# Kernel optimization log

Measured on AMD Instinct MI355X. Metric: run time of the kernel, lower is better.

Reference implementation:

```python
import jax, jax.numpy as jnp
import numpy as np

L_IN, L_K = 1, 1            # degree ranges (0..L)
C_IN, K_CH, H = 16, 8, 4    # in_channels, k_channels (per head), num_heads
C_OUT = H * K_CH            # 32
E, N_NODES, EMB = 32768, 4096, 64
M_IN, M_K = (L_IN + 1) ** 2, (L_K + 1) ** 2


def _so2_pairs(L_in, L_out):
    # enumerate SO(2)-equivariant weight blocks: for each order m, all (l_in, l_out)
    # pairs with l >= m; m=0 uses 1 matrix, m>0 uses 2 (real/imag parts).
    pairs, w = [], 0
    for m in range(min(L_in, L_out) + 1):
        for l_in in range(m, L_in + 1):
            for l_out in range(m, L_out + 1):
                pairs.append((m, l_in, l_out, w))
                w += 1 if m == 0 else 2
    return pairs, w

_PAIRS, NUM_W = _so2_pairs(L_IN, L_K)  # NUM_W = 6 for L_in=L_k=1


def so2_linear(x, W, L_in, L_out):
    # x: [E, (L_in+1)^2, Cin]; W: [NUM_W, Cin, Cout] (shared) or [E, NUM_W, Cin, Cout] (per-edge)
    per_edge = (W.ndim == 4)
    Cout = W.shape[-1]
    out = jnp.zeros((x.shape[0], (L_out + 1) ** 2, Cout), x.dtype)

    def mat(xs, w):
        return jnp.einsum('ec,eco->eo', xs, W[:, w]) if per_edge else xs @ W[w]

    pairs, _ = _so2_pairs(L_in, L_out)
    for m, l_in, l_out, w in pairs:
        i_in, i_out = l_in * (l_in + 1), l_out * (l_out + 1)  # flat index of (l, m=0)
        if m == 0:
            out = out.at[:, i_out].add(mat(x[:, i_in], w))
        else:
            xp, xn = x[:, i_in + m], x[:, i_in - m]
            out = out.at[:, i_out + m].add(mat(xp, w) - mat(xn, w + 1))
            out = out.at[:, i_out - m].add(mat(xp, w + 1) + mat(xn, w))
    return out


def segment_softmax(z, index, num_segments):
    # PyG-style softmax over ragged neighborhoods (max is detached, as in PyG)
    zmax = jax.lax.stop_gradient(jax.ops.segment_max(z, index, num_segments=num_segments))
    e = jnp.exp(z - zmax[index])
    denom = jax.ops.segment_sum(e, index, num_segments=num_segments)
    return e / denom[index]


def setup_inputs() -> dict:
    key = jax.random.key(0)
    ks = jax.random.split(key, 6)
    x_q = jax.random.normal(ks[0], (E, M_IN, C_IN), jnp.float32)
    x_k = jax.random.normal(ks[1], (E, M_IN, C_IN), jnp.float32)
    edge_emb = jax.random.normal(ks[2], (E, EMB), jnp.float32)
    index = jnp.sort(jax.random.randint(ks[3], (E,), 0, N_NODES))
    W_q = jax.random.normal(ks[4], (NUM_W, C_IN, C_OUT), jnp.float32) / np.sqrt(C_IN)
    W_p = jax.random.normal(ks[5], (EMB, NUM_W * C_IN * C_OUT), jnp.float32) / np.sqrt(EMB)
    return {"x_q": x_q, "x_k": x_k, "edge_emb": edge_emb, "index": index,
            "W_q": W_q, "W_p": W_p, "num_nodes": N_NODES}


def reference(x_q, x_k, edge_emb, index, W_q, W_p, num_nodes):
    # q_ij = W_Q x_i ; static SO2 weights
    q = so2_linear(x_q, W_q, L_IN, L_K).reshape(-1, M_K, H, K_CH)
    # k_ij = W_K(||r_ij||) x_j ; per-edge dynamic SO2 weights from edge embedding
    W_k = (edge_emb @ W_p).reshape(-1, NUM_W, C_IN, C_OUT)
    k = so2_linear(x_k, W_k, L_IN, L_K).reshape(-1, M_K, H, K_CH)
    scale = (K_CH // H) ** (-0.5)  # faithful to original: (k_channels // num_heads)**-0.5
    z = (q * k).sum((-1, -3)) * scale  # [E, H]
    return segment_softmax(z, index, num_nodes)
```

## Files before the change

### kernel.cpp

```cpp
#include <hip/hip_runtime.h>
#include <math.h>

#define E_TOTAL 32768
#define NUM_NODES 4096
#define SCALE 0.70710678118654752f

typedef __attribute__((ext_vector_type(8))) short bfrag;
typedef __attribute__((ext_vector_type(16))) float facc;

__device__ inline unsigned short f2bf(float f) {
  unsigned int u = __float_as_uint(f);
  unsigned int r = (u + 0x7FFFu + ((u >> 16) & 1u)) >> 16;
  return (unsigned short)r;
}
__device__ inline float bf2f(unsigned short s) {
  return __uint_as_float(((unsigned int)s) << 16);
}
__device__ inline void cvt8(const float* v, bfrag& hi, bfrag& lo) {
#pragma unroll
  for (int i = 0; i < 8; ++i) {
    unsigned short h = f2bf(v[i]);
    hi[i] = (short)h;
    lo[i] = (short)f2bf(v[i] - bf2f(h));
  }
}

__global__ __launch_bounds__(256) void prep_kernel(
    const float* __restrict__ Wp, const float* __restrict__ Wq,
    const int* __restrict__ index,
    unsigned short* __restrict__ fragWp, unsigned short* __restrict__ fragWq,
    int* __restrict__ offs)
{
  const int b = blockIdx.x, t = threadIdx.x;
  if (b < 96) {
    __shared__ unsigned short lds[4096];
    const int c = b / 6, w = b - c * 6;
    const int colbase = w * 512 + c * 32;
    const int cl = t & 31, dg = t >> 5;
#pragma unroll
    for (int i = 0; i < 8; ++i) {
      const int d = dg * 8 + i;
      const float v = Wp[(size_t)d * 3072 + colbase + cl];
      const unsigned short hi = f2bf(v);
      const unsigned short lo = f2bf(v - bf2f(hi));
      const int ks = d >> 4;
      const int lane = ((d >> 3) & 1) * 32 + cl;
      const int j = d & 7;
      lds[(ks * 2 + 0) * 512 + lane * 8 + j] = hi;
      lds[(ks * 2 + 1) * 512 + lane * 8 + j] = lo;
    }
    __syncthreads();
    unsigned short* dst = fragWp + (size_t)b * 4096;
    ((uint4*)dst)[t] = ((const uint4*)lds)[t];
    ((uint4*)dst)[t + 256] = ((const uint4*)lds)[t + 256];
  } else if (b < 103) {
    const int slot = b - 96;
    const int w = (slot == 6) ? 5 : slot;
    const float sgn = (slot == 6) ? -1.f : 1.f;
    for (int tt = t; tt < 512; tt += 256) {
      const int lane = tt >> 3, j = tt & 7;
      const int o = lane & 31, c = (lane >> 5) * 8 + j;
      const float v = sgn * Wq[(size_t)(w * 16 + c) * 32 + o];
      const unsigned short hi = f2bf(v);
      const unsigned short lo = f2bf(v - bf2f(hi));
      fragWq[slot * 1024 + lane * 8 + j] = hi;
      fragWq[slot * 1024 + 512 + lane * 8 + j] = lo;
    }
  } else {
    const int tg = (b - 103) * 256 + t;
    if (tg >= E_TOTAL) return;
    const int cur = index[tg];
    const int prev = (tg == 0) ? -1 : index[tg - 1];
    for (int n = prev + 1; n <= cur; ++n) offs[n] = tg;
    if (tg == E_TOTAL - 1)
      for (int n = cur + 1; n <= NUM_NODES; ++n) offs[n] = E_TOTAL;
  }
}

__global__ __launch_bounds__(256, 2) void main_kernel(
    const float* __restrict__ x_q, const float* __restrict__ x_k,
    const float* __restrict__ emb,
    const unsigned short* __restrict__ fragWp,
    const unsigned short* __restrict__ fragWq,
    float* __restrict__ z)
{
  __shared__ float xk_t[64][65];
  __shared__ float zred[4][32][4];

  const int t = threadIdx.x;
  const int lane = t & 63, wv = t >> 6;
  const int pr = wv & 1;
  const int col = lane & 31, half = lane >> 5;
  const int eb = blockIdx.x * 64;
  const int el = (wv >> 1) * 32 + col;
  const int e = eb + el;

  {
    const int er = t >> 2, dq = (t & 3) * 16;
    const float* src = x_k + (size_t)(eb + er) * 64 + dq;
#pragma unroll
    for (int i = 0; i < 4; ++i) {
      float4 v = *(const float4*)(src + i * 4);
      xk_t[dq + i * 4 + 0][er] = v.x;
      xk_t[dq + i * 4 + 1][er] = v.y;
      xk_t[dq + i * 4 + 2][er] = v.z;
      xk_t[dq + i * 4 + 3][er] = v.w;
    }
  }

  bfrag ebh[4], ebl[4];
#pragma unroll
  for (int ks = 0; ks < 4; ++ks) {
    float tmp[8];
    *(float4*)&tmp[0] = *(const float4*)(emb + (size_t)e * 64 + ks * 16 + half * 8);
    *(float4*)&tmp[4] = *(const float4*)(emb + (size_t)e * 64 + ks * 16 + half * 8 + 4);
    cvt8(tmp, ebh[ks], ebl[ks]);
  }

  facc ka0 = {0}, ka1 = {0}, ka2 = {0}, ka3 = {0};

  const unsigned short* fbase = fragWp + pr * 4096 + lane * 8;

  bfrag curh[4], curl[4], nxth[4], nxtl[4];
#pragma unroll
  for (int ks = 0; ks < 4; ++ks) {
    *(uint4*)&curh[ks] = *(const uint4*)(fbase + ks * 1024);
    *(uint4*)&curl[ks] = *(const uint4*)(fbase + ks * 1024 + 512);
  }

  __syncthreads();

  float xkc0 = 0.f, xkc1 = 0.f, xkc2 = 0.f, xkc3 = 0.f;

#pragma unroll 6
  for (int it = 0; it < 48; ++it) {
    const int j = it % 3;
    {
      const int itn = (it < 47) ? it + 1 : 47;
      const unsigned short* gp = fbase + (size_t)itn * 8192;
#pragma unroll
      for (int ks = 0; ks < 4; ++ks) {
        *(uint4*)&nxth[ks] = *(const uint4*)(gp + ks * 1024);
        *(uint4*)&nxtl[ks] = *(const uint4*)(gp + ks * 1024 + 512);
      }
    }
    if (j == 0) {
      const int c16 = it / 3;
      xkc0 = xk_t[c16][el];
      xkc1 = xk_t[16 + c16][el];
      xkc2 = xk_t[32 + c16][el];
      xkc3 = xk_t[48 + c16][el];
    }
    facc cc0 = {0.f}, cc1 = {0.f}, cc2 = {0.f};
#pragma unroll
    for (int ks = 0; ks < 4; ++ks) {
      cc0 = __builtin_amdgcn_mfma_f32_32x32x16_bf16(curh[ks], ebh[ks], cc0, 0, 0, 0);
      cc1 = __builtin_amdgcn_mfma_f32_32x32x16_bf16(curh[ks], ebl[ks], cc1, 0, 0, 0);
      cc2 = __builtin_amdgcn_mfma_f32_32x32x16_bf16(curl[ks], ebh[ks], cc2, 0, 0, 0);
    }
    if (j < 2) {
      const float xv = (j == 0) ? xkc0 : xkc2;
      if (pr == 0) {
#pragma unroll
        for (int r = 0; r < 16; ++r)
          ka0[r] = fmaf(xv, cc0[r] + cc1[r] + cc2[r], ka0[r]);
      } else {
#pragma unroll
        for (int r = 0; r < 16; ++r)
          ka2[r] = fmaf(xv, cc0[r] + cc1[r] + cc2[r], ka2[r]);
      }
    } else {
      if (pr == 0) {
#pragma unroll
        for (int r = 0; r < 16; ++r) {
          const float s = cc0[r] + cc1[r] + cc2[r];
          ka1[r] = fmaf(xkc1, s, ka1[r]);
          ka3[r] = fmaf(xkc3, s, ka3[r]);
        }
      } else {
#pragma unroll
        for (int r = 0; r < 16; ++r) {
          const float s = cc0[r] + cc1[r] + cc2[r];
          ka1[r] = fmaf(xkc3, s, ka1[r]);
          ka3[r] = fmaf(-xkc1, s, ka3[r]);
        }
      }
    }
#pragma unroll
    for (int ks = 0; ks < 4; ++ks) { curh[ks] = nxth[ks]; curl[ks] = nxtl[ks]; }
  }

  bfrag xqh[4], xql[4];
#pragma unroll
  for (int a = 0; a < 4; ++a) {
    float tmp[8];
    *(float4*)&tmp[0] = *(const float4*)(x_q + (size_t)e * 64 + a * 16 + half * 8);
    *(float4*)&tmp[4] = *(const float4*)(x_q + (size_t)e * 64 + a * 16 + half * 8 + 4);
    cvt8(tmp, xqh[a], xql[a]);
  }
  float zp0 = 0.f, zp1 = 0.f, zp2 = 0.f, zp3 = 0.f;
  const int QA1[4] = {0, 1, 0, 3}, QS1[4] = {0, 4, 1, 4};
  const int QA2[4] = {2, 3, 2, 1}, QS2[4] = {2, 5, 3, 6};
#pragma unroll
  for (int m = 0; m < 4; ++m) {
    facc qa = {0.f};
#pragma unroll
    for (int tm = 0; tm < 2; ++tm) {
      const int a = tm ? QA2[m] : QA1[m];
      const int sl = tm ? QS2[m] : QS1[m];
      bfrag wh, wl;
      *(uint4*)&wh = *(const uint4*)(fragWq + sl * 1024 + lane * 8);
      *(uint4*)&wl = *(const uint4*)(fragWq + sl * 1024 + 512 + lane * 8);
      qa = __builtin_amdgcn_mfma_f32_32x32x16_bf16(wh, xqh[a], qa, 0, 0, 0);
      qa = __builtin_amdgcn_mfma_f32_32x32x16_bf16(wh, xql[a], qa, 0, 0, 0);
      qa = __builtin_amdgcn_mfma_f32_32x32x16_bf16(wl, xqh[a], qa, 0, 0, 0);
    }
    const facc& km = (m == 0) ? ka0 : (m == 1) ? ka1 : (m == 2) ? ka2 : ka3;
#pragma unroll
    for (int r = 0; r < 16; ++r) {
      const float v = qa[r] * km[r];
      if (r < 4) zp0 += v;
      else if (r < 8) zp1 += v;
      else if (r < 12) zp2 += v;
      else zp3 += v;
    }
  }
  zp0 += __shfl_xor(zp0, 32);
  zp1 += __shfl_xor(zp1, 32);
  zp2 += __shfl_xor(zp2, 32);
  zp3 += __shfl_xor(zp3, 32);
  if (half == 0) {
    float4 v = {zp0, zp1, zp2, zp3};
    *(float4*)&zred[wv][col][0] = v;
  }
  __syncthreads();
  if (pr == 0 && half == 0) {
    float4 a = *(const float4*)&zred[wv][col][0];
    float4 b = *(const float4*)&zred[wv ^ 1][col][0];
    float4 o = {(a.x + b.x) * SCALE, (a.y + b.y) * SCALE,
                (a.z + b.z) * SCALE, (a.w + b.w) * SCALE};
    *(float4*)&z[(size_t)e * 4] = o;
  }
}

__global__ __launch_bounds__(256) void softmax_kernel(
    const float* __restrict__ z, const int* __restrict__ offs,
    float* __restrict__ out)
{
  const int node = blockIdx.x * 4 + (threadIdx.x >> 6);
  const int lane = threadIdx.x & 63;
  const int start = offs[node], end = offs[node + 1];
  if (start >= end) return;
  const int h = lane & 3, eo = lane >> 2;
  float m = -INFINITY;
  for (int e = start + eo; e < end; e += 16) m = fmaxf(m, z[(size_t)e * 4 + h]);
#pragma unroll
  for (int s = 4; s < 64; s <<= 1) m = fmaxf(m, __shfl_xor(m, s));
  float sum = 0.f;
  for (int e = start + eo; e < end; e += 16) sum += __expf(z[(size_t)e * 4 + h] - m);
#pragma unroll
  for (int s = 4; s < 64; s <<= 1) sum += __shfl_xor(sum, s);
  const float inv = 1.f / sum;
  for (int e = start + eo; e < end; e += 16)
    out[(size_t)e * 4 + h] = __expf(z[(size_t)e * 4 + h] - m) * inv;
}

extern "C" void kernel_launch(void* const* d_in, const int* in_sizes, int n_in,
                              void* d_out, int out_size, void* d_ws, size_t ws_size,
                              hipStream_t stream) {
  const float* x_q = (const float*)d_in[0];
  const float* x_k = (const float*)d_in[1];
  const float* emb = (const float*)d_in[2];
  const int* index = (const int*)d_in[3];
  const float* W_q = (const float*)d_in[4];
  const float* W_p = (const float*)d_in[5];
  float* out = (float*)d_out;

  char* ws = (char*)d_ws;
  float* z = (float*)ws;
  int* offs = (int*)(ws + 524288);
  unsigned short* fragWp = (unsigned short*)(ws + 524288 + 32768);
  unsigned short* fragWq = (unsigned short*)(ws + 524288 + 32768 + 786432);

  prep_kernel<<<231, 256, 0, stream>>>(W_p, W_q, index, fragWp, fragWq, offs);
  main_kernel<<<512, 256, 0, stream>>>(x_q, x_k, emb, fragWp, fragWq, z);
  softmax_kernel<<<1024, 256, 0, stream>>>(z, offs, out);
}
```

Measured before the change: 123.9 us.

## Split per-edge weight channel loop across eight waves and drop offsets pass

Doubles the main kernel block to 512 threads. Each wave pair now covers all 32 output columns for 32 edges, and four wave groups split the 16 input channels among them, so each wave runs 24 iterations instead of 48. Partial z values are reduced across the four groups through shared memory. Separately, the segment-offset computation is removed from the prep kernel and the softmax kernel finds each node's edge range by binary search on the sorted index. This adds redundant index reads and a larger cross-wave reduction, and raises register pressure under the 512x4 launch bounds.

```diff
diff --git a/kernel.cpp b/kernel.cpp
--- a/kernel.cpp
+++ b/kernel.cpp
@@ -27,9 +27,7 @@
 
 __global__ __launch_bounds__(256) void prep_kernel(
     const float* __restrict__ Wp, const float* __restrict__ Wq,
-    const int* __restrict__ index,
-    unsigned short* __restrict__ fragWp, unsigned short* __restrict__ fragWq,
-    int* __restrict__ offs)
+    unsigned short* __restrict__ fragWp, unsigned short* __restrict__ fragWq)
 {
   const int b = blockIdx.x, t = threadIdx.x;
   if (b < 96) {
@@ -53,7 +51,7 @@
     unsigned short* dst = fragWp + (size_t)b * 4096;
     ((uint4*)dst)[t] = ((const uint4*)lds)[t];
     ((uint4*)dst)[t + 256] = ((const uint4*)lds)[t + 256];
-  } else if (b < 103) {
+  } else {
     const int slot = b - 96;
     const int w = (slot == 6) ? 5 : slot;
     const float sgn = (slot == 6) ? -1.f : 1.f;
@@ -66,18 +64,10 @@
       fragWq[slot * 1024 + lane * 8 + j] = hi;
       fragWq[slot * 1024 + 512 + lane * 8 + j] = lo;
     }
-  } else {
-    const int tg = (b - 103) * 256 + t;
-    if (tg >= E_TOTAL) return;
-    const int cur = index[tg];
-    const int prev = (tg == 0) ? -1 : index[tg - 1];
-    for (int n = prev + 1; n <= cur; ++n) offs[n] = tg;
-    if (tg == E_TOTAL - 1)
-      for (int n = cur + 1; n <= NUM_NODES; ++n) offs[n] = E_TOTAL;
-  }
-}
-
-__global__ __launch_bounds__(256, 2) void main_kernel(
+  }
+}
+
+__global__ __launch_bounds__(512, 4) void main_kernel(
     const float* __restrict__ x_q, const float* __restrict__ x_k,
     const float* __restrict__ emb,
     const unsigned short* __restrict__ fragWp,
@@ -85,27 +75,25 @@
     float* __restrict__ z)
 {
   __shared__ float xk_t[64][65];
-  __shared__ float zred[4][32][4];
+  __shared__ float zred[8][32][4];
 
   const int t = threadIdx.x;
   const int lane = t & 63, wv = t >> 6;
-  const int pr = wv & 1;
+  const int pg = wv & 1, cr = wv >> 1;
   const int col = lane & 31, half = lane >> 5;
   const int eb = blockIdx.x * 64;
-  const int el = (wv >> 1) * 32 + col;
+  const int el = pg * 32 + col;
   const int e = eb + el;
 
   {
-    const int er = t >> 2, dq = (t & 3) * 16;
+    const int er = t >> 3, dq = (t & 7) * 8;
     const float* src = x_k + (size_t)(eb + er) * 64 + dq;
-#pragma unroll
-    for (int i = 0; i < 4; ++i) {
-      float4 v = *(const float4*)(src + i * 4);
-      xk_t[dq + i * 4 + 0][er] = v.x;
-      xk_t[dq + i * 4 + 1][er] = v.y;
-      xk_t[dq + i * 4 + 2][er] = v.z;
-      xk_t[dq + i * 4 + 3][er] = v.w;
-    }
+    float4 v0 = *(const float4*)(src);
+    float4 v1 = *(const float4*)(src + 4);
+    xk_t[dq + 0][er] = v0.x; xk_t[dq + 1][er] = v0.y;
+    xk_t[dq + 2][er] = v0.z; xk_t[dq + 3][er] = v0.w;
+    xk_t[dq + 4][er] = v1.x; xk_t[dq + 5][er] = v1.y;
+    xk_t[dq + 6][er] = v1.z; xk_t[dq + 7][er] = v1.w;
   }
 
   bfrag ebh[4], ebl[4];
@@ -119,13 +107,16 @@
 
   facc ka0 = {0}, ka1 = {0}, ka2 = {0}, ka3 = {0};
 
-  const unsigned short* fbase = fragWp + pr * 4096 + lane * 8;
+  const unsigned short* fbase = fragWp + lane * 8;
 
   bfrag curh[4], curl[4], nxth[4], nxtl[4];
-#pragma unroll
-  for (int ks = 0; ks < 4; ++ks) {
-    *(uint4*)&curh[ks] = *(const uint4*)(fbase + ks * 1024);
-    *(uint4*)&curl[ks] = *(const uint4*)(fbase + ks * 1024 + 512);
+  {
+    const unsigned short* gp = fbase + (size_t)(cr * 6) * 4096;
+#pragma unroll
+    for (int ks = 0; ks < 4; ++ks) {
+      *(uint4*)&curh[ks] = *(const uint4*)(gp + ks * 1024);
+      *(uint4*)&curl[ks] = *(const uint4*)(gp + ks * 1024 + 512);
+    }
   }
 
   __syncthreads();
@@ -133,23 +124,25 @@
   float xkc0 = 0.f, xkc1 = 0.f, xkc2 = 0.f, xkc3 = 0.f;
 
 #pragma unroll 6
-  for (int it = 0; it < 48; ++it) {
-    const int j = it % 3;
+  for (int idx = 0; idx < 24; ++idx) {
+    const int w = idx % 6;
     {
-      const int itn = (it < 47) ? it + 1 : 47;
-      const unsigned short* gp = fbase + (size_t)itn * 8192;
+      const int nidx = (idx < 23) ? idx + 1 : 23;
+      const int nc = cr + 4 * (nidx / 6);
+      const int nw = nidx - 6 * (nidx / 6);
+      const unsigned short* gp = fbase + (size_t)(nc * 6 + nw) * 4096;
 #pragma unroll
       for (int ks = 0; ks < 4; ++ks) {
         *(uint4*)&nxth[ks] = *(const uint4*)(gp + ks * 1024);
         *(uint4*)&nxtl[ks] = *(const uint4*)(gp + ks * 1024 + 512);
       }
     }
-    if (j == 0) {
-      const int c16 = it / 3;
-      xkc0 = xk_t[c16][el];
-      xkc1 = xk_t[16 + c16][el];
-      xkc2 = xk_t[32 + c16][el];
-      xkc3 = xk_t[48 + c16][el];
+    if (w == 0) {
+      const int c = cr + 4 * (idx / 6);
+      xkc0 = xk_t[c][el];
+      xkc1 = xk_t[16 + c][el];
+      xkc2 = xk_t[32 + c][el];
+      xkc3 = xk_t[48 + c][el];
     }
     facc cc0 = {0.f}, cc1 = {0.f}, cc2 = {0.f};
 #pragma unroll
@@ -158,32 +151,31 @@
       cc1 = __builtin_amdgcn_mfma_f32_32x32x16_bf16(curh[ks], ebl[ks], cc1, 0, 0, 0);
       cc2 = __builtin_amdgcn_mfma_f32_32x32x16_bf16(curl[ks], ebh[ks], cc2, 0, 0, 0);
     }
-    if (j < 2) {
-      const float xv = (j == 0) ? xkc0 : xkc2;
-      if (pr == 0) {
-#pragma unroll
-        for (int r = 0; r < 16; ++r)
-          ka0[r] = fmaf(xv, cc0[r] + cc1[r] + cc2[r], ka0[r]);
-      } else {
-#pragma unroll
-        for (int r = 0; r < 16; ++r)
-          ka2[r] = fmaf(xv, cc0[r] + cc1[r] + cc2[r], ka2[r]);
+    if (w == 0) {
+#pragma unroll
+      for (int r = 0; r < 16; ++r) ka0[r] = fmaf(xkc0, cc0[r] + cc1[r] + cc2[r], ka0[r]);
+    } else if (w == 1) {
+#pragma unroll
+      for (int r = 0; r < 16; ++r) ka2[r] = fmaf(xkc0, cc0[r] + cc1[r] + cc2[r], ka2[r]);
+    } else if (w == 2) {
+#pragma unroll
+      for (int r = 0; r < 16; ++r) ka0[r] = fmaf(xkc2, cc0[r] + cc1[r] + cc2[r], ka0[r]);
+    } else if (w == 3) {
+#pragma unroll
+      for (int r = 0; r < 16; ++r) ka2[r] = fmaf(xkc2, cc0[r] + cc1[r] + cc2[r], ka2[r]);
+    } else if (w == 4) {
+#pragma unroll
+      for (int r = 0; r < 16; ++r) {
+        const float s = cc0[r] + cc1[r] + cc2[r];
+        ka1[r] = fmaf(xkc1, s, ka1[r]);
+        ka3[r] = fmaf(xkc3, s, ka3[r]);
       }
     } else {
-      if (pr == 0) {
-#pragma unroll
-        for (int r = 0; r < 16; ++r) {
-          const float s = cc0[r] + cc1[r] + cc2[r];
-          ka1[r] = fmaf(xkc1, s, ka1[r]);
-          ka3[r] = fmaf(xkc3, s, ka3[r]);
-        }
-      } else {
-#pragma unroll
-        for (int r = 0; r < 16; ++r) {
-          const float s = cc0[r] + cc1[r] + cc2[r];
-          ka1[r] = fmaf(xkc3, s, ka1[r]);
-          ka3[r] = fmaf(-xkc1, s, ka3[r]);
-        }
+#pragma unroll
+      for (int r = 0; r < 16; ++r) {
+        const float s = cc0[r] + cc1[r] + cc2[r];
+        ka1[r] = fmaf(xkc3, s, ka1[r]);
+        ka3[r] = fmaf(-xkc1, s, ka3[r]);
       }
     }
 #pragma unroll
@@ -234,22 +226,31 @@
     *(float4*)&zred[wv][col][0] = v;
   }
   __syncthreads();
-  if (pr == 0 && half == 0) {
-    float4 a = *(const float4*)&zred[wv][col][0];
-    float4 b = *(const float4*)&zred[wv ^ 1][col][0];
-    float4 o = {(a.x + b.x) * SCALE, (a.y + b.y) * SCALE,
-                (a.z + b.z) * SCALE, (a.w + b.w) * SCALE};
+  if (cr == 0 && half == 0) {
+    float4 a = *(const float4*)&zred[pg][col][0];
+    float4 b = *(const float4*)&zred[pg + 2][col][0];
+    float4 c4 = *(const float4*)&zred[pg + 4][col][0];
+    float4 d4 = *(const float4*)&zred[pg + 6][col][0];
+    float4 o = {(a.x + b.x + c4.x + d4.x) * SCALE,
+                (a.y + b.y + c4.y + d4.y) * SCALE,
+                (a.z + b.z + c4.z + d4.z) * SCALE,
+                (a.w + b.w + c4.w + d4.w) * SCALE};
     *(float4*)&z[(size_t)e * 4] = o;
   }
 }
 
 __global__ __launch_bounds__(256) void softmax_kernel(
-    const float* __restrict__ z, const int* __restrict__ offs,
+    const float* __restrict__ z, const int* __restrict__ index,
     float* __restrict__ out)
 {
   const int node = blockIdx.x * 4 + (threadIdx.x >> 6);
   const int lane = threadIdx.x & 63;
-  const int start = offs[node], end = offs[node + 1];
+  int lo = 0, hi = E_TOTAL;
+  while (lo < hi) { int mid = (lo + hi) >> 1; if (index[mid] < node) lo = mid + 1; else hi = mid; }
+  const int start = lo;
+  hi = E_TOTAL;
+  while (lo < hi) { int mid = (lo + hi) >> 1; if (index[mid] < node + 1) lo = mid + 1; else hi = mid; }
+  const int end = lo;
   if (start >= end) return;
   const int h = lane & 3, eo = lane >> 2;
   float m = -INFINITY;
@@ -278,11 +279,10 @@
 
   char* ws = (char*)d_ws;
   float* z = (float*)ws;
-  int* offs = (int*)(ws + 524288);
-  unsigned short* fragWp = (unsigned short*)(ws + 524288 + 32768);
-  unsigned short* fragWq = (unsigned short*)(ws + 524288 + 32768 + 786432);
-
-  prep_kernel<<<231, 256, 0, stream>>>(W_p, W_q, index, fragWp, fragWq, offs);
-  main_kernel<<<512, 256, 0, stream>>>(x_q, x_k, emb, fragWp, fragWq, z);
-  softmax_kernel<<<1024, 256, 0, stream>>>(z, offs, out);
-}
+  unsigned short* fragWp = (unsigned short*)(ws + 524288);
+  unsigned short* fragWq = (unsigned short*)(ws + 524288 + 786432);
+
+  prep_kernel<<<103, 256, 0, stream>>>(W_p, W_q, fragWp, fragWq);
+  main_kernel<<<512, 512, 0, stream>>>(x_q, x_k, emb, fragWp, fragWq, z);
+  softmax_kernel<<<1024, 256, 0, stream>>>(z, index, out);
+}
```

New measurement: 436.7 us. +252.3%, slower.
